# Performance work log

Hardware: AMD Instinct MI355X
Metric: run time of the kernel (lower is better)

Reference implementation:

```python
import jax, jax.numpy as jnp
import numpy as np

OBJ_DIM, REL_DIM, EFF_DIM = 5, 1, 100
REL_HID, OBJ_HID, OUT_DIM = 150, 100, 2


def _init_linear(key, fan_in, fan_out):
    kw, kb = jax.random.split(key)
    bound = 1.0 / np.sqrt(fan_in)
    W = jax.random.uniform(kw, (fan_in, fan_out), jnp.float32, -bound, bound)
    b = jax.random.uniform(kb, (fan_out,), jnp.float32, -bound, bound)
    return W, b


def setup_inputs() -> dict:
    key = jax.random.key(0)
    ks = jax.random.split(key, 12)
    B, N, R = 64, 100, 9900
    inp = {
        "objects": jax.random.normal(ks[0], (B, N, OBJ_DIM), jnp.float32),
        "sender_relations": jax.random.uniform(ks[1], (B, N, R), jnp.float32),
        "receiver_relations": jax.random.uniform(ks[2], (B, N, R), jnp.float32),
        "relation_info": jax.random.normal(ks[3], (B, R, REL_DIM), jnp.float32),
    }
    # relational MLP: (2*obj + rel) -> 150 -> 150 -> effect_dim, ReLU after each
    rW1, rb1 = _init_linear(ks[4], 2 * OBJ_DIM + REL_DIM, REL_HID)
    rW2, rb2 = _init_linear(ks[5], REL_HID, REL_HID)
    rW3, rb3 = _init_linear(ks[6], REL_HID, EFF_DIM)
    # object MLP: (obj + effect) -> 100 -> 100 -> 2
    oW1, ob1 = _init_linear(ks[7], OBJ_DIM + EFF_DIM, OBJ_HID)
    oW2, ob2 = _init_linear(ks[8], OBJ_HID, OBJ_HID)
    oW3, ob3 = _init_linear(ks[9], OBJ_HID, OUT_DIM)
    inp.update(rW1=rW1, rb1=rb1, rW2=rW2, rb2=rb2, rW3=rW3, rb3=rb3,
               oW1=oW1, ob1=ob1, oW2=oW2, ob2=ob2, oW3=oW3, ob3=ob3)
    return inp


def _relational_mlp(x, rW1, rb1, rW2, rb2, rW3, rb3):
    h = jax.nn.relu(x @ rW1 + rb1)
    h = jax.nn.relu(h @ rW2 + rb2)
    return jax.nn.relu(h @ rW3 + rb3)


def _object_mlp(x, oW1, ob1, oW2, ob2, oW3, ob3):
    h = jax.nn.relu(x @ oW1 + ob1)
    h = jax.nn.relu(h @ oW2 + ob2)
    return h @ oW3 + ob3


def reference(objects, sender_relations, receiver_relations, relation_info,
              rW1, rb1, rW2, rb2, rW3, rb3, oW1, ob1, oW2, ob2, oW3, ob3):
    # gather: [B,R,N] @ [B,N,D] -> [B,R,D]
    senders = jnp.einsum('bnr,bnd->brd', sender_relations, objects)
    receivers = jnp.einsum('bnr,bnd->brd', receiver_relations, objects)
    rel_in = jnp.concatenate([senders, receivers, relation_info], axis=2)
    effects = _relational_mlp(rel_in, rW1, rb1, rW2, rb2, rW3, rb3)  # [B,R,E]
    # scatter: [B,N,R] @ [B,R,E] -> [B,N,E]
    effect_receivers = jnp.einsum('bnr,bre->bne', receiver_relations, effects)
    obj_in = jnp.concatenate([objects, effect_receivers], axis=2)
    return _object_mlp(obj_in, oW1, ob1, oW2, ob2, oW3, ob3)  # [B,N,2]
```

## Files before the change

kernel.cpp:

```cpp
#include <hip/hip_runtime.h>
#include <hip/hip_bf16.h>

#define B_    64
#define N_    100
#define R_    9900
#define OBJD  5
#define EFF   100

typedef __bf16 bf16x8 __attribute__((ext_vector_type(8)));
typedef float  f32x4  __attribute__((ext_vector_type(4)));

__device__ __forceinline__ ushort f2bf(float f) {
    union { float f; unsigned u; } x; x.f = f;
    unsigned r = x.u + 0x7fffu + ((x.u >> 16) & 1u);
    return (ushort)(r >> 16);
}
__device__ __forceinline__ float bf2f(ushort u) {
    union { unsigned u; float f; } x; x.u = ((unsigned)u) << 16;
    return x.f;
}

#define WTR_OBJ 52096

__global__ __launch_bounds__(256) void k_prepw(
    const float* __restrict__ W1, const float* __restrict__ W2,
    const float* __restrict__ W3, const float* __restrict__ O1,
    const float* __restrict__ O2, const float* __restrict__ O3,
    ushort* __restrict__ WTR)
{
    const int img = blockIdx.x;
    if (img == 0) {
        for (int idx = threadIdx.x; idx < 6400; idx += 256) {
            const int c = idx / 40, k = idx - (idx/40)*40;
            WTR[idx] = f2bf((c < 150 && k < 11) ? W1[k*150 + c] : 0.f);
        }
    } else if (img == 1) {
        for (int idx = threadIdx.x; idx < 26880; idx += 256) {
            const int c = idx / 168, k = idx - (idx/168)*168;
            WTR[6400 + idx] = f2bf((c < 150 && k < 150) ? W2[k*150 + c] : 0.f);
        }
    } else if (img == 2) {
        for (int idx = threadIdx.x; idx < 18816; idx += 256) {
            const int c = idx / 168, k = idx - (idx/168)*168;
            WTR[33280 + idx] = f2bf((c < 100 && k < 150) ? W3[k*100 + c] : 0.f);
        }
    } else {
        const int j = img - 3;
        ushort* dst = WTR + WTR_OBJ + (size_t)j*11520;
        for (int idx = threadIdx.x; idx < 11520; idx += 256) {
            const int cc = idx / 72, kk = idx - (idx/72)*72;
            float v = 0.f;
            if (kk < 64) {
                if (j < 4) {
                    const int kg = j*64 + kk;
                    int row = -1;
                    if (kg < 5) row = kg;
                    else if (kg >= 8 && kg < 108) row = kg - 3;
                    else if (kg >= 108 && kg < 208) row = kg - 103;
                    if (cc < 100 && row >= 0) v = O1[row*100 + cc];
                } else if (j < 6) {
                    const int kg = (j-4)*64 + kk;
                    if (cc < 100 && kg < 100) v = O2[kg*100 + cc];
                } else {
                    const int kg = (j-6)*64 + kk;
                    if (cc < 2 && kg < 100) v = O3[kg*2 + cc];
                }
            }
            dst[idx] = f2bf(v);
        }
    }
}

#define LW1 0
#define LW2 6400
#define LW3 33280
#define LBA 52096
#define LBB 60160
#define LACT 68224
#define LBIAS 78976
#define LTOT 79776

__global__ __launch_bounds__(512, 1) void k_relmlp_p(
    const float* __restrict__ obj, const float* __restrict__ SR,
    const float* __restrict__ RR, const float* __restrict__ RI,
    const ushort* __restrict__ WTR,
    const float* __restrict__ b1, const float* __restrict__ b2,
    const float* __restrict__ b3, float* __restrict__ ER)
{
    __shared__ __align__(16) ushort lds[LTOT];
    const int t  = threadIdx.x;
    const int b  = blockIdx.x >> 2;
    const int qt = blockIdx.x & 3;
    const int lane = t & 63, w = t >> 6;
    const int lo = lane & 15, hi = lane >> 4;
    const int mt = w & 3, nh = w >> 2;
    const int q  = t & 7,  rr = t >> 3;

    #pragma unroll
    for (int j = 0; j < 13; ++j) {
        const int idx = t + j*512;
        if (idx < 6512)
            reinterpret_cast<uint4*>(lds)[idx] =
                reinterpret_cast<const uint4*>(WTR)[idx];
    }
    {
        float* bias_w = (float*)(lds + LBIAS);
        if (t < 150)      bias_w[t] = b1[t];
        else if (t < 300) bias_w[t] = b2[t-150];
        else if (t < 400) bias_w[t] = b3[t-300];
    }
    if (t < 216) {
        ushort* base = lds + ((t < 108) ? LBA : LBB) + 100*72;
        const int k = (t < 108) ? t : t - 108;
        *reinterpret_cast<uint4*>(base + k*8) = make_uint4(0u, 0u, 0u, 0u);
    }

    float objv[13][5];
    {
        const int n0 = q*13;
        #pragma unroll
        for (int i = 0; i < 13; ++i) {
            const int n = n0 + i;
            #pragma unroll
            for (int d = 0; d < 5; ++d)
                objv[i][d] = (n < N_) ? obj[(size_t)b*500 + n*5 + d] : 0.f;
        }
    }

    const int tile0 = qt*39;
    const int tile1 = (tile0 + 39 < 155) ? tile0 + 39 : 155;

    ushort* bufA = lds + LBA;
    ushort* bufB = lds + LBB;
    ushort* act  = lds + LACT;
    const float* bias = (const float*)(lds + LBIAS);

    f32x4 acc_er[7];
    #pragma unroll
    for (int ct = 0; ct < 7; ++ct) acc_er[ct] = (f32x4){0.f, 0.f, 0.f, 0.f};

    float4 psr[4], prr[4];
    float pri = 0.f, pri_n = 0.f;
    auto load4 = [&](float4* p, const float* M, int tile) {
        const int rr0 = tile*64;
        const int nr = (R_ - rr0 < 64) ? R_ - rr0 : 64;
        #pragma unroll
        for (int i = 0; i < 4; ++i) {
            const int idx = t + i*512;
            const int ci = idx < 1600 ? idx : 1599;
            const int n = ci >> 4, qq = ci & 15;
            const int col = (qq*4 < nr) ? qq*4 : 0;
            p[i] = *reinterpret_cast<const float4*>(
                &M[((size_t)b*N_ + n)*R_ + rr0 + col]);
        }
    };
    auto store4 = [&](const float4* p, ushort* dst, int nrow) {
        #pragma unroll
        for (int i = 0; i < 4; ++i) {
            const int idx = t + i*512;
            if (idx < 1600) {
                const int n = idx >> 4, qq = idx & 15;
                float4 v = p[i];
                if (qq*4 >= nrow) v = make_float4(0.f, 0.f, 0.f, 0.f);
                *reinterpret_cast<ushort4*>(&dst[n*72 + qq*4]) =
                    make_ushort4(f2bf(v.x), f2bf(v.y), f2bf(v.z), f2bf(v.w));
            }
        }
    };
    auto loadRI = [&](int tile) -> float {
        const int rr0 = tile*64;
        return (t < 64 && rr0 + t < R_) ? RI[(size_t)b*R_ + rr0 + t] : 0.f;
    };

    load4(psr, SR, tile0);
    load4(prr, RR, tile0);
    pri = loadRI(tile0);
    __syncthreads();

    for (int tile = tile0; tile < tile1; ++tile) {
        const int r0 = tile*64;
        const int nrow = (R_ - r0 < 64) ? R_ - r0 : 64;

        store4(psr, bufA, nrow);
        store4(prr, bufB, nrow);
        if (tile + 1 < tile1) {
            load4(psr, SR, tile+1);
            load4(prr, RR, tile+1);
            pri_n = loadRI(tile+1);
        }
        __syncthreads();

        {
            float s0=0.f,s1=0.f,s2=0.f,s3=0.f,s4=0.f;
            float g0=0.f,g1=0.f,g2=0.f,g3=0.f,g4=0.f;
            const int n0 = q*13;
            #pragma unroll
            for (int i = 0; i < 13; ++i) {
                const int n = n0 + i;
                const float ms = bf2f(bufA[n*72 + rr]);
                const float mr = bf2f(bufB[n*72 + rr]);
                s0 += ms*objv[i][0]; s1 += ms*objv[i][1]; s2 += ms*objv[i][2];
                s3 += ms*objv[i][3]; s4 += ms*objv[i][4];
                g0 += mr*objv[i][0]; g1 += mr*objv[i][1]; g2 += mr*objv[i][2];
                g3 += mr*objv[i][3]; g4 += mr*objv[i][4];
            }
            #pragma unroll
            for (int msk = 1; msk < 8; msk <<= 1) {
                s0 += __shfl_xor(s0, msk); s1 += __shfl_xor(s1, msk);
                s2 += __shfl_xor(s2, msk); s3 += __shfl_xor(s3, msk);
                s4 += __shfl_xor(s4, msk);
                g0 += __shfl_xor(g0, msk); g1 += __shfl_xor(g1, msk);
                g2 += __shfl_xor(g2, msk); g3 += __shfl_xor(g3, msk);
                g4 += __shfl_xor(g4, msk);
            }
            if (q < 5) {
                const float sv = (q==0)?s0:(q==1)?s1:(q==2)?s2:(q==3)?s3:s4;
                const float gv = (q==0)?g0:(q==1)?g1:(q==2)?g2:(q==3)?g3:g4;
                act[rr*168 + q]     = f2bf(sv);
                act[rr*168 + 5 + q] = f2bf(gv);
            }
            if (t < 64) {
                act[t*168 + 10] = f2bf(pri);
                act[t*168 + 11] = 0;
            } else if (t < 128) {
                const int rz = t - 64;
                #pragma unroll
                for (int p = 0; p < 5; ++p)
                    *reinterpret_cast<ushort4*>(&act[rz*168 + 12 + p*4]) =
                        make_ushort4(0,0,0,0);
            }
            pri = pri_n;
        }
        __syncthreads();

        {
            f32x4 acc[5];
            #pragma unroll
            for (int j = 0; j < 5; ++j) {
                const int c = (nh*5 + j)*16 + lo;
                const float bv = (c < 150) ? bias[c] : 0.f;
                acc[j][0]=bv; acc[j][1]=bv; acc[j][2]=bv; acc[j][3]=bv;
            }
            const bf16x8 a = *reinterpret_cast<const bf16x8*>(
                &act[(mt*16 + lo)*168 + hi*8]);
            #pragma unroll
            for (int j = 0; j < 5; ++j) {
                const int ct = nh*5 + j;
                const bf16x8 bb = *reinterpret_cast<const bf16x8*>(
                    &lds[LW1 + (ct*16 + lo)*40 + hi*8]);
                acc[j] = __builtin_amdgcn_mfma_f32_16x16x32_bf16(a, bb, acc[j], 0,0,0);
            }
            __syncthreads();
            #pragma unroll
            for (int j = 0; j < 5; ++j) {
                const int ct = nh*5 + j;
                #pragma unroll
                for (int r = 0; r < 4; ++r)
                    act[(mt*16 + hi*4 + r)*168 + ct*16 + lo] =
                        f2bf(fmaxf(acc[j][r], 0.f));
            }
            __syncthreads();
        }
        {
            f32x4 acc[5];
            #pragma unroll
            for (int j = 0; j < 5; ++j) {
                const int c = (nh*5 + j)*16 + lo;
                const float bv = (c < 150) ? bias[150 + c] : 0.f;
                acc[j][0]=bv; acc[j][1]=bv; acc[j][2]=bv; acc[j][3]=bv;
            }
            #pragma unroll
            for (int ks = 0; ks < 5; ++ks) {
                const bf16x8 a = *reinterpret_cast<const bf16x8*>(
                    &act[(mt*16 + lo)*168 + ks*32 + hi*8]);
                #pragma unroll
                for (int j = 0; j < 5; ++j) {
                    const int ct = nh*5 + j;
                    const bf16x8 bb = *reinterpret_cast<const bf16x8*>(
                        &lds[LW2 + (ct*16 + lo)*168 + ks*32 + hi*8]);
                    acc[j] = __builtin_amdgcn_mfma_f32_16x16x32_bf16(a, bb, acc[j], 0,0,0);
                }
            }
            __syncthreads();
            #pragma unroll
            for (int j = 0; j < 5; ++j) {
                const int ct = nh*5 + j;
                #pragma unroll
                for (int r = 0; r < 4; ++r)
                    act[(mt*16 + hi*4 + r)*168 + ct*16 + lo] =
                        f2bf(fmaxf(acc[j][r], 0.f));
            }
            __syncthreads();
        }
        {
            const int nct = nh ? 3 : 4;
            f32x4 acc[4];
            #pragma unroll
            for (int j = 0; j < 4; ++j) {
                const int c = (nh*4 + j)*16 + lo;
                const float bv = (c < 100) ? bias[300 + c] : 0.f;
                acc[j][0]=bv; acc[j][1]=bv; acc[j][2]=bv; acc[j][3]=bv;
            }
            #pragma unroll
            for (int ks = 0; ks < 5; ++ks) {
                const bf16x8 a = *reinterpret_cast<const bf16x8*>(
                    &act[(mt*16 + lo)*168 + ks*32 + hi*8]);
                #pragma unroll
                for (int j = 0; j < 4; ++j) {
                    if (j < nct) {
                        const int ct = nh*4 + j;
                        const bf16x8 bb = *reinterpret_cast<const bf16x8*>(
                            &lds[LW3 + (ct*16 + lo)*168 + ks*32 + hi*8]);
                        acc[j] = __builtin_amdgcn_mfma_f32_16x16x32_bf16(a, bb, acc[j], 0,0,0);
                    }
                }
            }
            #pragma unroll
            for (int j = 0; j < 4; ++j) {
                if (j < nct) {
                    const int e = (nh*4 + j)*16 + lo;
                    if (e < 100) {
                        ushort4 o;
                        o.x = f2bf(fmaxf(acc[j][0], 0.f));
                        o.y = f2bf(fmaxf(acc[j][1], 0.f));
                        o.z = f2bf(fmaxf(acc[j][2], 0.f));
                        o.w = f2bf(fmaxf(acc[j][3], 0.f));
                        *reinterpret_cast<ushort4*>(&bufA[e*72 + mt*16 + hi*4]) = o;
                    }
                }
            }
            __syncthreads();
        }

        if (w < 7) {
            #pragma unroll
            for (int ks = 0; ks < 2; ++ks) {
                const bf16x8 a = *reinterpret_cast<const bf16x8*>(
                    &bufB[(w*16 + lo)*72 + ks*32 + hi*8]);
                #pragma unroll
                for (int ct = 0; ct < 7; ++ct) {
                    const bf16x8 bb = *reinterpret_cast<const bf16x8*>(
                        &bufA[(ct*16 + lo)*72 + ks*32 + hi*8]);
                    acc_er[ct] = __builtin_amdgcn_mfma_f32_16x16x32_bf16(
                        a, bb, acc_er[ct], 0, 0, 0);
                }
            }
        }
        __syncthreads();
    }

    if (w < 7) {
        #pragma unroll
        for (int ct = 0; ct < 7; ++ct) {
            const int e = ct*16 + lo;
            if (e < EFF) {
                #pragma unroll
                for (int rg = 0; rg < 4; ++rg) {
                    const int n = w*16 + hi*4 + rg;
                    if (n < N_)
                        atomicAdd(&ER[((size_t)b*N_ + n)*EFF + e], acc_er[ct][rg]);
                }
            }
        }
    }
}

__device__ __forceinline__ void img_load(const ushort* __restrict__ g,
                                         uint4* pre, int t) {
    #pragma unroll
    for (int j = 0; j < 6; ++j) {
        int idx = t + j*256;
        int cidx = idx < 1440 ? idx : 1439;
        pre[j] = *reinterpret_cast<const uint4*>(g + (size_t)cidx*8);
    }
}
__device__ __forceinline__ void img_store(const uint4* pre, ushort* wt, int t) {
    #pragma unroll
    for (int j = 0; j < 6; ++j) {
        int idx = t + j*256;
        if (idx < 1440)
            *reinterpret_cast<uint4*>(wt + (size_t)idx*8) = pre[j];
    }
}

template<int COUT, int NCHUNK, int LASTKS, int NCT, bool RELU, int EPI, int ASTR>
__device__ __forceinline__ void mfma_layerO(
    const ushort* __restrict__ WT, const float* __restrict__ Bias,
    ushort* act, ushort* wt, int t, float* gout, int grow0)
{
    const int lane = t & 63;
    const int wv   = t >> 6;
    const int lo   = lane & 15;
    const int hi   = lane >> 4;

    f32x4 acc[2][NCT];
    #pragma unroll
    for (int ct = 0; ct < NCT; ++ct) {
        const int c = ct*16 + lo;
        const float bv = (c < COUT) ? Bias[c] : 0.f;
        #pragma unroll
        for (int m = 0; m < 2; ++m) {
            acc[m][ct][0] = bv; acc[m][ct][1] = bv;
            acc[m][ct][2] = bv; acc[m][ct][3] = bv;
        }
    }

    uint4 pre[6];
    img_load(WT, pre, t);
    #pragma unroll
    for (int q = 0; q < NCHUNK; ++q) {
        __syncthreads();
        img_store(pre, wt, t);
        if (q + 1 < NCHUNK) img_load(WT + (size_t)(q+1)*11520, pre, t);
        __syncthreads();
        const int nks = (q == NCHUNK-1) ? LASTKS : 2;
        #pragma unroll
        for (int ks = 0; ks < 2; ++ks) {
            if (ks < nks) {
                const int kg = q*64 + ks*32;
                const bf16x8 a0 = *reinterpret_cast<const bf16x8*>(
                    &act[(wv*32 +      lo)*ASTR + kg + hi*8]);
                const bf16x8 a1 = *reinterpret_cast<const bf16x8*>(
                    &act[(wv*32 + 16 + lo)*ASTR + kg + hi*8]);
                #pragma unroll
                for (int ct = 0; ct < NCT; ++ct) {
                    const bf16x8 b = *reinterpret_cast<const bf16x8*>(
                        &wt[(ct*16 + lo)*72 + ks*32 + hi*8]);
                    acc[0][ct] = __builtin_amdgcn_mfma_f32_16x16x32_bf16(
                        a0, b, acc[0][ct], 0, 0, 0);
                    acc[1][ct] = __builtin_amdgcn_mfma_f32_16x16x32_bf16(
                        a1, b, acc[1][ct], 0, 0, 0);
                }
            }
        }
    }

    __syncthreads();
    if (EPI == 0) {
        #pragma unroll
        for (int m = 0; m < 2; ++m)
            #pragma unroll
            for (int ct = 0; ct < NCT; ++ct)
                #pragma unroll
                for (int r = 0; r < 4; ++r) {
                    float v = acc[m][ct][r];
                    if (RELU) v = fmaxf(v, 0.f);
                    act[(wv*32 + m*16 + hi*4 + r)*ASTR + ct*16 + lo] = f2bf(v);
                }
    } else {
        #pragma unroll
        for (int m = 0; m < 2; ++m)
            #pragma unroll
            for (int r = 0; r < 4; ++r)
                if (lo < 2)
                    gout[(size_t)(grow0 + wv*32 + m*16 + hi*4 + r)*2 + lo] =
                        acc[m][0][r];
    }
    __syncthreads();
}

#define OSTR 232

__global__ __launch_bounds__(256, 1) void k_objmlp_mfma(
    const float* __restrict__ obj, const float* __restrict__ ER,
    const ushort* __restrict__ WO,
    const float* __restrict__ ob1, const float* __restrict__ ob2,
    const float* __restrict__ ob3, float* __restrict__ out)
{
    __shared__ __align__(16) ushort act[128*OSTR];
    __shared__ __align__(16) ushort wt[160*72];
    const int t = threadIdx.x;
    const int rowbase = blockIdx.x * 128;

    float4 per[13];
    #pragma unroll
    for (int j = 0; j < 13; ++j) {
        const int idx = t + j*256;
        const int ci = idx < 3200 ? idx : 3199;
        const int row = ci / 25, c = ci - row*25;
        per[j] = *reinterpret_cast<const float4*>(
            &ER[(size_t)(rowbase + row)*100 + c*4]);
    }
    #pragma unroll
    for (int j = 0; j < 13; ++j) {
        const int idx = t + j*256;
        if (idx < 3200) {
            const int row = idx / 25, c = idx - row*25;
            ushort h[4], l[4];
            #pragma unroll
            for (int k = 0; k < 4; ++k) {
                const float f = ((const float*)&per[j])[k];
                h[k] = f2bf(f);
                l[k] = f2bf(f - bf2f(h[k]));
            }
            *reinterpret_cast<ushort4*>(&act[row*OSTR + 8 + c*4]) =
                make_ushort4(h[0], h[1], h[2], h[3]);
            *reinterpret_cast<ushort4*>(&act[row*OSTR + 108 + c*4]) =
                make_ushort4(l[0], l[1], l[2], l[3]);
        }
    }
    #pragma unroll
    for (int j = 0; j < 3; ++j) {
        const int idx = t + j*256;
        if (idx < 640) {
            const int row = idx / 5, d = idx - row*5;
            act[row*OSTR + d] = f2bf(obj[(size_t)(rowbase + row)*5 + d]);
        }
    }
    #pragma unroll
    for (int j = 0; j < 2; ++j) {
        const int idx = t + j*256;
        if (idx < 384) {
            const int row = idx / 3, c = 5 + (idx - row*3);
            act[row*OSTR + c] = 0;
        }
    }
    #pragma unroll
    for (int j = 0; j < 2; ++j) {
        const int idx = t + j*256;
        if (idx < 512) {
            const int row = idx >> 2, p = idx & 3;
            *reinterpret_cast<ushort4*>(&act[row*OSTR + 208 + p*4]) =
                make_ushort4(0, 0, 0, 0);
        }
    }

    mfma_layerO<100, 4, 1, 7, true,  0, OSTR>(WO,           ob1, act, wt, t, nullptr, 0);
    mfma_layerO<100, 2, 2, 7, true,  0, OSTR>(WO + 4*11520, ob2, act, wt, t, nullptr, 0);
    mfma_layerO<2,   2, 2, 1, false, 2, OSTR>(WO + 6*11520, ob3, act, wt, t, out, rowbase);
}

extern "C" void kernel_launch(void* const* d_in, const int* in_sizes, int n_in,
                              void* d_out, int out_size, void* d_ws, size_t ws_size,
                              hipStream_t stream)
{
    const float* objects = (const float*)d_in[0];
    const float* SR      = (const float*)d_in[1];
    const float* RR      = (const float*)d_in[2];
    const float* RI      = (const float*)d_in[3];
    const float* rW1 = (const float*)d_in[4];  const float* rb1 = (const float*)d_in[5];
    const float* rW2 = (const float*)d_in[6];  const float* rb2 = (const float*)d_in[7];
    const float* rW3 = (const float*)d_in[8];  const float* rb3 = (const float*)d_in[9];
    const float* oW1 = (const float*)d_in[10]; const float* ob1 = (const float*)d_in[11];
    const float* oW2 = (const float*)d_in[12]; const float* ob2 = (const float*)d_in[13];
    const float* oW3 = (const float*)d_in[14]; const float* ob3 = (const float*)d_in[15];
    float* out = (float*)d_out;

    char* ws = (char*)d_ws;
    float*  ER  = (float*)ws;
    ushort* WTR = (ushort*)(ws + (size_t)B_*N_*EFF*4);

    hipMemsetAsync(ER, 0, (size_t)B_*N_*EFF*sizeof(float), stream);

    k_prepw<<<dim3(11), 256, 0, stream>>>(rW1, rW2, rW3, oW1, oW2, oW3, WTR);

    k_relmlp_p<<<dim3(256), 512, 0, stream>>>(objects, SR, RR, RI, WTR,
                                              rb1, rb2, rb3, ER);

    k_objmlp_mfma<<<dim3(50), 256, 0, stream>>>(objects, ER, WTR + WTR_OBJ,
                                                ob1, ob2, ob3, out);
}
```

Measured before the change: 398.4 us.

## Replace ER atomics with per-quarter partial buffers and drop a barrier

Each of the four R-quarter blocks now writes its partial effect sums to its own ER slice with plain stores. The object MLP sums the four slices on load, which removes the memset and the atomicAdd traffic. The gather result moves to a separate small LDS buffer, so the layer-1 MFMA no longer needs a barrier before act is overwritten. The code also switches to hardware bf16 conversion with packed pair stores. The cost is four times the ER workspace and more global reads in the object kernel.

```diff
diff --git a/kernel.cpp b/kernel.cpp
--- a/kernel.cpp
+++ b/kernel.cpp
@@ -8,12 +8,17 @@
 #define EFF   100
 
 typedef __bf16 bf16x8 __attribute__((ext_vector_type(8)));
+typedef __bf16 bf16x2 __attribute__((ext_vector_type(2)));
+typedef short  short8v __attribute__((ext_vector_type(8)));
 typedef float  f32x4  __attribute__((ext_vector_type(4)));
 
 __device__ __forceinline__ ushort f2bf(float f) {
-    union { float f; unsigned u; } x; x.f = f;
-    unsigned r = x.u + 0x7fffu + ((x.u >> 16) & 1u);
-    return (ushort)(r >> 16);
+    __bf16 h = (__bf16)f;
+    return __builtin_bit_cast(ushort, h);
+}
+__device__ __forceinline__ unsigned pk2(float a, float b) {
+    bf16x2 v; v[0] = (__bf16)a; v[1] = (__bf16)b;
+    return __builtin_bit_cast(unsigned, v);
 }
 __device__ __forceinline__ float bf2f(ushort u) {
     union { unsigned u; float f; } x; x.u = ((unsigned)u) << 16;
@@ -78,7 +83,8 @@
 #define LBB 60160
 #define LACT 68224
 #define LBIAS 78976
-#define LTOT 79776
+#define LGB  79776
+#define LTOT 81312
 
 __global__ __launch_bounds__(512, 1) void k_relmlp_p(
     const float* __restrict__ obj, const float* __restrict__ SR,
@@ -114,6 +120,13 @@
         const int k = (t < 108) ? t : t - 108;
         *reinterpret_cast<uint4*>(base + k*8) = make_uint4(0u, 0u, 0u, 0u);
     }
+    if (t < 64) {
+        ushort* gb0 = lds + LGB + t*24;
+        gb0[11] = 0;
+        *reinterpret_cast<ushort4*>(&gb0[12]) = make_ushort4(0,0,0,0);
+        *reinterpret_cast<ushort4*>(&gb0[16]) = make_ushort4(0,0,0,0);
+        *reinterpret_cast<ushort4*>(&gb0[20]) = make_ushort4(0,0,0,0);
+    }
 
     float objv[13][5];
     {
@@ -133,6 +146,7 @@
     ushort* bufA = lds + LBA;
     ushort* bufB = lds + LBB;
     ushort* act  = lds + LACT;
+    ushort* gb   = lds + LGB;
     const float* bias = (const float*)(lds + LBIAS);
 
     f32x4 acc_er[7];
@@ -162,8 +176,8 @@
                 const int n = idx >> 4, qq = idx & 15;
                 float4 v = p[i];
                 if (qq*4 >= nrow) v = make_float4(0.f, 0.f, 0.f, 0.f);
-                *reinterpret_cast<ushort4*>(&dst[n*72 + qq*4]) =
-                    make_ushort4(f2bf(v.x), f2bf(v.y), f2bf(v.z), f2bf(v.w));
+                uint2 u; u.x = pk2(v.x, v.y); u.y = pk2(v.z, v.w);
+                *reinterpret_cast<uint2*>(&dst[n*72 + qq*4]) = u;
             }
         }
     };
@@ -216,19 +230,10 @@
             if (q < 5) {
                 const float sv = (q==0)?s0:(q==1)?s1:(q==2)?s2:(q==3)?s3:s4;
                 const float gv = (q==0)?g0:(q==1)?g1:(q==2)?g2:(q==3)?g3:g4;
-                act[rr*168 + q]     = f2bf(sv);
-                act[rr*168 + 5 + q] = f2bf(gv);
-            }
-            if (t < 64) {
-                act[t*168 + 10] = f2bf(pri);
-                act[t*168 + 11] = 0;
-            } else if (t < 128) {
-                const int rz = t - 64;
-                #pragma unroll
-                for (int p = 0; p < 5; ++p)
-                    *reinterpret_cast<ushort4*>(&act[rz*168 + 12 + p*4]) =
-                        make_ushort4(0,0,0,0);
-            }
+                gb[rr*24 + q]     = f2bf(sv);
+                gb[rr*24 + 5 + q] = f2bf(gv);
+            }
+            if (t < 64) gb[t*24 + 10] = f2bf(pri);
             pri = pri_n;
         }
         __syncthreads();
@@ -241,8 +246,10 @@
                 const float bv = (c < 150) ? bias[c] : 0.f;
                 acc[j][0]=bv; acc[j][1]=bv; acc[j][2]=bv; acc[j][3]=bv;
             }
-            const bf16x8 a = *reinterpret_cast<const bf16x8*>(
-                &act[(mt*16 + lo)*168 + hi*8]);
+            bf16x8 a = __builtin_bit_cast(bf16x8, (short8v)0);
+            if (hi < 2)
+                a = *reinterpret_cast<const bf16x8*>(
+                    &gb[(mt*16 + lo)*24 + hi*8]);
             #pragma unroll
             for (int j = 0; j < 5; ++j) {
                 const int ct = nh*5 + j;
@@ -250,7 +257,6 @@
                     &lds[LW1 + (ct*16 + lo)*40 + hi*8]);
                 acc[j] = __builtin_amdgcn_mfma_f32_16x16x32_bf16(a, bb, acc[j], 0,0,0);
             }
-            __syncthreads();
             #pragma unroll
             for (int j = 0; j < 5; ++j) {
                 const int ct = nh*5 + j;
@@ -320,12 +326,10 @@
                 if (j < nct) {
                     const int e = (nh*4 + j)*16 + lo;
                     if (e < 100) {
-                        ushort4 o;
-                        o.x = f2bf(fmaxf(acc[j][0], 0.f));
-                        o.y = f2bf(fmaxf(acc[j][1], 0.f));
-                        o.z = f2bf(fmaxf(acc[j][2], 0.f));
-                        o.w = f2bf(fmaxf(acc[j][3], 0.f));
-                        *reinterpret_cast<ushort4*>(&bufA[e*72 + mt*16 + hi*4]) = o;
+                        uint2 u;
+                        u.x = pk2(fmaxf(acc[j][0], 0.f), fmaxf(acc[j][1], 0.f));
+                        u.y = pk2(fmaxf(acc[j][2], 0.f), fmaxf(acc[j][3], 0.f));
+                        *reinterpret_cast<uint2*>(&bufA[e*72 + mt*16 + hi*4]) = u;
                     }
                 }
             }
@@ -350,6 +354,7 @@
     }
 
     if (w < 7) {
+        float* ERq = ER + ((size_t)qt*B_ + b)*(size_t)(N_*EFF);
         #pragma unroll
         for (int ct = 0; ct < 7; ++ct) {
             const int e = ct*16 + lo;
@@ -358,7 +363,7 @@
                 for (int rg = 0; rg < 4; ++rg) {
                     const int n = w*16 + hi*4 + rg;
                     if (n < N_)
-                        atomicAdd(&ER[((size_t)b*N_ + n)*EFF + e], acc_er[ct][rg]);
+                        ERq[n*EFF + e] = acc_er[ct][rg];
                 }
             }
         }
@@ -460,6 +465,7 @@
 }
 
 #define OSTR 232
+#define ERSL ((size_t)B_*N_*EFF)
 
 __global__ __launch_bounds__(256, 1) void k_objmlp_mfma(
     const float* __restrict__ obj, const float* __restrict__ ER,
@@ -478,8 +484,15 @@
         const int idx = t + j*256;
         const int ci = idx < 3200 ? idx : 3199;
         const int row = ci / 25, c = ci - row*25;
-        per[j] = *reinterpret_cast<const float4*>(
-            &ER[(size_t)(rowbase + row)*100 + c*4]);
+        const float* p = &ER[(size_t)(rowbase + row)*100 + c*4];
+        const float4 a0 = *reinterpret_cast<const float4*>(p);
+        const float4 a1 = *reinterpret_cast<const float4*>(p + ERSL);
+        const float4 a2 = *reinterpret_cast<const float4*>(p + 2*ERSL);
+        const float4 a3 = *reinterpret_cast<const float4*>(p + 3*ERSL);
+        per[j] = make_float4(a0.x + a1.x + a2.x + a3.x,
+                             a0.y + a1.y + a2.y + a3.y,
+                             a0.z + a1.z + a2.z + a3.z,
+                             a0.w + a1.w + a2.w + a3.w);
     }
     #pragma unroll
     for (int j = 0; j < 13; ++j) {
@@ -547,16 +560,14 @@
     float* out = (float*)d_out;
 
     char* ws = (char*)d_ws;
-    float*  ER  = (float*)ws;
-    ushort* WTR = (ushort*)(ws + (size_t)B_*N_*EFF*4);
-
-    hipMemsetAsync(ER, 0, (size_t)B_*N_*EFF*sizeof(float), stream);
+    float*  ERp = (float*)ws;
+    ushort* WTR = (ushort*)(ws + (size_t)4*B_*N_*EFF*sizeof(float));
 
     k_prepw<<<dim3(11), 256, 0, stream>>>(rW1, rW2, rW3, oW1, oW2, oW3, WTR);
 
     k_relmlp_p<<<dim3(256), 512, 0, stream>>>(objects, SR, RR, RI, WTR,
-                                              rb1, rb2, rb3, ER);
-
-    k_objmlp_mfma<<<dim3(50), 256, 0, stream>>>(objects, ER, WTR + WTR_OBJ,
+                                              rb1, rb2, rb3, ERp);
+
+    k_objmlp_mfma<<<dim3(50), 256, 0, stream>>>(objects, ERp, WTR + WTR_OBJ,
                                                 ob1, ob2, ob3, out);
 }
```

Result: faster. 366.9 us (-7.9%).
